# Kernel tuning notes

Measured on AMD Instinct MI355X. Metric: run time of the kernel, lower is better.

The kernel has to match this reference:

```python
import jax, jax.numpy as jnp
import numpy as np

B, S, H, D = 4, 1024, 16, 64


def setup_inputs() -> dict:
    key = jax.random.key(0)
    k1, k2 = jax.random.split(key)
    qkv = jax.random.normal(k1, (B, S, 3, H, D), dtype=jnp.float32)
    bias = jax.random.normal(k2, (1, H, S, S), dtype=jnp.float32)
    return {"qkv": qkv, "bias": bias}


def reference(qkv, bias):
    # flash_attn_qkvpacked_func(qkv, softmax_scale=None -> 1/sqrt(D), bias=bias, causal=False)
    q = qkv[:, :, 0]  # (B, S, H, D)
    k = qkv[:, :, 1]
    v = qkv[:, :, 2]
    scale = 1.0 / jnp.sqrt(jnp.asarray(D, dtype=qkv.dtype))
    # scores: (B, H, S_q, S_k)
    scores = jnp.einsum("bshd,bthd->bhst", q, k) * scale + bias
    probs = jax.nn.softmax(scores, axis=-1)
    out = jnp.einsum("bhst,bthd->bshd", probs, v)  # (B, S, H, D)
    return out
```

## Files before the change

kernel.cpp:

```cpp
#include <hip/hip_runtime.h>

#define NB 4
#define NS 1024
#define NH 16
#define ND 64

typedef __attribute__((ext_vector_type(8))) short bf16x8;
typedef __attribute__((ext_vector_type(4))) float f32x4;

static __device__ __forceinline__ short f2bf(float x) {
  __bf16 h = (__bf16)x;
  return __builtin_bit_cast(short, h);
}
static __device__ __forceinline__ float bf2f(short s) {
  unsigned u = ((unsigned)(unsigned short)s) << 16;
  return __builtin_bit_cast(float, u);
}

__global__ __launch_bounds__(512, 2)
void fsa_fwd(const float* __restrict__ qkv,
             const float* __restrict__ bias,
             float* __restrict__ out)
{
  const int hw = blockIdx.x;
  const int lg = ((hw & 7) << 6) | (hw >> 3);
  const int b  = lg & 3;
  const int qt = (lg >> 2) & 7;
  const int h  = lg >> 5;

  const int tid  = threadIdx.x;
  const int w    = tid >> 6;
  const int lane = tid & 63;
  const int lo   = lane & 15;
  const int hi   = lane >> 4;
  const int q0   = qt * 128;

  __shared__ __attribute__((aligned(16))) short Ksh[64 * 64];
  __shared__ __attribute__((aligned(16))) short VTsh[64 * 64];
  __shared__ __attribute__((aligned(16))) short Psh[8][16 * 64];

  bf16x8 qf[2];
  {
    const int qs = q0 + w * 16 + lo;
    const float* qp = qkv + ((size_t)(b * NS + qs) * 3) * (NH * ND) + h * ND + hi * 8;
    #pragma unroll
    for (int f = 0; f < 2; ++f) {
      float4 x0 = *(const float4*)(qp + f * 32);
      float4 x1 = *(const float4*)(qp + f * 32 + 4);
      float v[8] = {x0.x, x0.y, x0.z, x0.w, x1.x, x1.y, x1.z, x1.w};
      #pragma unroll
      for (int j = 0; j < 8; ++j) qf[f][j] = f2bf(v[j] * 0.125f);
    }
  }

  const size_t tstr = 3 * NH * ND;
  const float* kg = qkv + (size_t)b * NS * tstr + 1 * NH * ND + h * ND;
  const float* vg = qkv + (size_t)b * NS * tstr + 2 * NH * ND + h * ND;

  const int krow = tid >> 3;
  const int kd   = (tid & 7) * 8;
  const int vrow = (tid & 31) * 2;
  const int vd   = (tid >> 5) * 4;

  const float* bb = bias + (size_t)h * NS * NS + (size_t)(q0 + w * 16 + hi * 4) * NS + lo;

  float psum[4] = {0.f, 0.f, 0.f, 0.f};
  f32x4 oacc[4];
  #pragma unroll
  for (int dt = 0; dt < 4; ++dt) { f32x4 z = {0.f, 0.f, 0.f, 0.f}; oacc[dt] = z; }

  for (int it = 0; it < 16; ++it) {
    const int t0 = it * 64;

    bf16x8 w0;
    {
      const float* src = kg + (size_t)(t0 + krow) * tstr + kd;
      float4 a = ((const float4*)src)[0];
      float4 c = ((const float4*)src)[1];
      float v[8] = {a.x,a.y,a.z,a.w, c.x,c.y,c.z,c.w};
      #pragma unroll
      for (int j = 0; j < 8; ++j) w0[j] = f2bf(v[j]);
    }
    unsigned vpk[4];
    {
      const float* s0 = vg + (size_t)(t0 + vrow) * tstr + vd;
      const float* s1 = s0 + tstr;
      float4 a0 = *(const float4*)s0;
      float4 b0 = *(const float4*)s1;
      float r0[4] = {a0.x,a0.y,a0.z,a0.w};
      float r1[4] = {b0.x,b0.y,b0.z,b0.w};
      #pragma unroll
      for (int j = 0; j < 4; ++j)
        vpk[j] = (unsigned)(unsigned short)f2bf(r0[j]) |
                 ((unsigned)(unsigned short)f2bf(r1[j]) << 16);
    }

    __syncthreads();

    {
      const int base = krow * 64 + kd;
      const int sw = (krow & 7) << 3;
      *(bf16x8*)&Ksh[(base ^ sw)] = w0;
    }
    {
      unsigned* vt32 = (unsigned*)VTsh;
      #pragma unroll
      for (int j = 0; j < 4; ++j) {
        const int R = vd + j;
        vt32[R * 32 + ((vrow >> 1) ^ ((R & 7) << 2))] = vpk[j];
      }
    }

    float br[4][4];
    #pragma unroll
    for (int r = 0; r < 4; ++r)
      #pragma unroll
      for (int tt = 0; tt < 4; ++tt)
        br[r][tt] = bb[(size_t)r * NS + t0 + tt * 16];

    __syncthreads();

    __builtin_amdgcn_s_setprio(1);
    f32x4 sacc[4];
    #pragma unroll
    for (int tt = 0; tt < 4; ++tt) {
      f32x4 sb;
      #pragma unroll
      for (int r = 0; r < 4; ++r) sb[r] = br[r][tt] - 8.f;
      const int kr = tt * 16 + lo;
      const int ksw = (kr & 7) << 3;
      bf16x8 k0 = *(const bf16x8*)&Ksh[(kr * 64      + hi * 8) ^ ksw];
      bf16x8 k1 = *(const bf16x8*)&Ksh[(kr * 64 + 32 + hi * 8) ^ ksw];
      sb = __builtin_amdgcn_mfma_f32_16x16x32_bf16(qf[0], k0, sb, 0, 0, 0);
      sb = __builtin_amdgcn_mfma_f32_16x16x32_bf16(qf[1], k1, sb, 0, 0, 0);
      sacc[tt] = sb;
    }

    short* pw = Psh[w];
    #pragma unroll
    for (int r = 0; r < 4; ++r) {
      const int row = hi * 4 + r;
      const int sw = (row & 7) << 3;
      #pragma unroll
      for (int tt = 0; tt < 4; ++tt) {
        float p = __expf(sacc[tt][r]);
        short pb = f2bf(p);
        psum[r] += bf2f(pb);
        pw[row * 64 + ((tt * 16 + lo) ^ sw)] = pb;
      }
    }
    asm volatile("s_waitcnt lgkmcnt(0)" ::: "memory");

    bf16x8 pf0, pf1;
    {
      const int psw = (lo & 7) << 3;
      pf0 = *(const bf16x8*)&pw[lo * 64 + ((     hi * 8) ^ psw)];
      pf1 = *(const bf16x8*)&pw[lo * 64 + ((32 + hi * 8) ^ psw)];
    }
    #pragma unroll
    for (int dt = 0; dt < 4; ++dt) {
      const int vr = dt * 16 + lo;
      const int vsw = (vr & 7) << 3;
      bf16x8 v0 = *(const bf16x8*)&VTsh[vr * 64 + ((     hi * 8) ^ vsw)];
      bf16x8 v1 = *(const bf16x8*)&VTsh[vr * 64 + ((32 + hi * 8) ^ vsw)];
      oacc[dt] = __builtin_amdgcn_mfma_f32_16x16x32_bf16(pf0, v0, oacc[dt], 0, 0, 0);
      oacc[dt] = __builtin_amdgcn_mfma_f32_16x16x32_bf16(pf1, v1, oacc[dt], 0, 0, 0);
    }
    __builtin_amdgcn_s_setprio(0);
  }

  #pragma unroll
  for (int r = 0; r < 4; ++r) {
    psum[r] += __shfl_xor(psum[r], 1, 64);
    psum[r] += __shfl_xor(psum[r], 2, 64);
    psum[r] += __shfl_xor(psum[r], 4, 64);
    psum[r] += __shfl_xor(psum[r], 8, 64);
  }

  float* ob = out + ((size_t)(b * NS + q0 + w * 16 + hi * 4) * NH + h) * ND + lo;
  #pragma unroll
  for (int r = 0; r < 4; ++r) {
    float inv = 1.f / psum[r];
    #pragma unroll
    for (int dt = 0; dt < 4; ++dt)
      ob[(size_t)r * NH * ND + dt * 16] = oacc[dt][r] * inv;
  }
}

extern "C" void kernel_launch(void* const* d_in, const int* in_sizes, int n_in,
                              void* d_out, int out_size, void* d_ws, size_t ws_size,
                              hipStream_t stream) {
  const float* qkv  = (const float*)d_in[0];
  const float* bias = (const float*)d_in[1];
  float* out = (float*)d_out;
  dim3 grid(NB * NH * (NS / 128));
  fsa_fwd<<<grid, 512, 0, stream>>>(qkv, bias, out);
}
```

Measured before the change: 49.22 us.

## Prefetch next K/V and bias tile into registers, switch softmax to exp2

Global loads for the next K/V tile and the next bias tile are now issued into registers during the current iteration, so their latency overlaps the current MFMA and softmax work. Q is prescaled by log2(e) and the bias is scaled the same way, so the exponential becomes a native exp2. The row sum now accumulates fp32 probabilities instead of their bf16-rounded values. This keeps more registers live under launch_bounds(512,2) and slightly changes the rounding of the normalisation.

Measured after the change: 64.67 us. 31.4% more time.

```diff
diff --git a/kernel.cpp b/kernel.cpp
--- a/kernel.cpp
+++ b/kernel.cpp
@@ -1,4 +1,5 @@
 #include <hip/hip_runtime.h>
+#include <cmath>
 
 #define NB 4
 #define NS 1024
@@ -12,10 +13,16 @@
   __bf16 h = (__bf16)x;
   return __builtin_bit_cast(short, h);
 }
-static __device__ __forceinline__ float bf2f(short s) {
-  unsigned u = ((unsigned)(unsigned short)s) << 16;
-  return __builtin_bit_cast(float, u);
-}
+
+static __device__ __forceinline__ float fast_exp2(float x) {
+#if __has_builtin(__builtin_amdgcn_exp2f)
+  return __builtin_amdgcn_exp2f(x);
+#else
+  return exp2f(x);
+#endif
+}
+
+#define LOG2E 1.44269504f
 
 __global__ __launch_bounds__(512, 2)
 void fsa_fwd(const float* __restrict__ qkv,
@@ -49,7 +56,7 @@
       float4 x1 = *(const float4*)(qp + f * 32 + 4);
       float v[8] = {x0.x, x0.y, x0.z, x0.w, x1.x, x1.y, x1.z, x1.w};
       #pragma unroll
-      for (int j = 0; j < 8; ++j) qf[f][j] = f2bf(v[j] * 0.125f);
+      for (int j = 0; j < 8; ++j) qf[f][j] = f2bf(v[j] * (0.125f * LOG2E));
     }
   }
 
@@ -69,71 +76,81 @@
   #pragma unroll
   for (int dt = 0; dt < 4; ++dt) { f32x4 z = {0.f, 0.f, 0.f, 0.f}; oacc[dt] = z; }
 
+  float4 kpa, kpb, vpa, vpb;
+  float br[4][4];
+
+#define LOAD_KV(T0) do { \
+    const float* src_ = kg + (size_t)((T0) + krow) * tstr + kd; \
+    kpa = ((const float4*)src_)[0]; \
+    kpb = ((const float4*)src_)[1]; \
+    const float* s0_ = vg + (size_t)((T0) + vrow) * tstr + vd; \
+    vpa = *(const float4*)s0_; \
+    vpb = *(const float4*)(s0_ + tstr); \
+  } while (0)
+
+#define LOAD_BIAS(T0) do { \
+    _Pragma("unroll") \
+    for (int r_ = 0; r_ < 4; ++r_) { \
+      _Pragma("unroll") \
+      for (int tt_ = 0; tt_ < 4; ++tt_) \
+        br[r_][tt_] = bb[(size_t)r_ * NS + (T0) + tt_ * 16]; \
+    } \
+  } while (0)
+
+#define STAGE() do { \
+    bf16x8 w0_; \
+    { \
+      float v_[8] = {kpa.x,kpa.y,kpa.z,kpa.w, kpb.x,kpb.y,kpb.z,kpb.w}; \
+      _Pragma("unroll") \
+      for (int j_ = 0; j_ < 8; ++j_) w0_[j_] = f2bf(v_[j_]); \
+    } \
+    { \
+      const int base_ = krow * 64 + kd; \
+      const int sw_ = (krow & 7) << 3; \
+      *(bf16x8*)&Ksh[base_ ^ sw_] = w0_; \
+    } \
+    { \
+      float r0_[4] = {vpa.x,vpa.y,vpa.z,vpa.w}; \
+      float r1_[4] = {vpb.x,vpb.y,vpb.z,vpb.w}; \
+      unsigned* vt_ = (unsigned*)VTsh; \
+      _Pragma("unroll") \
+      for (int j_ = 0; j_ < 4; ++j_) { \
+        unsigned pk_ = (unsigned)(unsigned short)f2bf(r0_[j_]) | \
+                       ((unsigned)(unsigned short)f2bf(r1_[j_]) << 16); \
+        const int R_ = vd + j_; \
+        vt_[R_ * 32 + ((vrow >> 1) ^ ((R_ & 7) << 2))] = pk_; \
+      } \
+    } \
+  } while (0)
+
+  LOAD_KV(0);
+  LOAD_BIAS(0);
+
+  #pragma unroll 1
   for (int it = 0; it < 16; ++it) {
-    const int t0 = it * 64;
-
-    bf16x8 w0;
-    {
-      const float* src = kg + (size_t)(t0 + krow) * tstr + kd;
-      float4 a = ((const float4*)src)[0];
-      float4 c = ((const float4*)src)[1];
-      float v[8] = {a.x,a.y,a.z,a.w, c.x,c.y,c.z,c.w};
+    __syncthreads();
+    STAGE();
+    if (it < 15) LOAD_KV((it + 1) * 64);
+    __syncthreads();
+
+    f32x4 sacc[4];
+    #pragma unroll
+    for (int tt = 0; tt < 4; ++tt) {
       #pragma unroll
-      for (int j = 0; j < 8; ++j) w0[j] = f2bf(v[j]);
-    }
-    unsigned vpk[4];
-    {
-      const float* s0 = vg + (size_t)(t0 + vrow) * tstr + vd;
-      const float* s1 = s0 + tstr;
-      float4 a0 = *(const float4*)s0;
-      float4 b0 = *(const float4*)s1;
-      float r0[4] = {a0.x,a0.y,a0.z,a0.w};
-      float r1[4] = {b0.x,b0.y,b0.z,b0.w};
-      #pragma unroll
-      for (int j = 0; j < 4; ++j)
-        vpk[j] = (unsigned)(unsigned short)f2bf(r0[j]) |
-                 ((unsigned)(unsigned short)f2bf(r1[j]) << 16);
-    }
-
-    __syncthreads();
-
-    {
-      const int base = krow * 64 + kd;
-      const int sw = (krow & 7) << 3;
-      *(bf16x8*)&Ksh[(base ^ sw)] = w0;
-    }
-    {
-      unsigned* vt32 = (unsigned*)VTsh;
-      #pragma unroll
-      for (int j = 0; j < 4; ++j) {
-        const int R = vd + j;
-        vt32[R * 32 + ((vrow >> 1) ^ ((R & 7) << 2))] = vpk[j];
-      }
-    }
-
-    float br[4][4];
-    #pragma unroll
-    for (int r = 0; r < 4; ++r)
-      #pragma unroll
-      for (int tt = 0; tt < 4; ++tt)
-        br[r][tt] = bb[(size_t)r * NS + t0 + tt * 16];
-
-    __syncthreads();
+      for (int r = 0; r < 4; ++r)
+        sacc[tt][r] = br[r][tt] * LOG2E - (8.f * LOG2E);
+    }
+    if (it < 15) LOAD_BIAS((it + 1) * 64);
 
     __builtin_amdgcn_s_setprio(1);
-    f32x4 sacc[4];
     #pragma unroll
     for (int tt = 0; tt < 4; ++tt) {
-      f32x4 sb;
-      #pragma unroll
-      for (int r = 0; r < 4; ++r) sb[r] = br[r][tt] - 8.f;
       const int kr = tt * 16 + lo;
       const int ksw = (kr & 7) << 3;
       bf16x8 k0 = *(const bf16x8*)&Ksh[(kr * 64      + hi * 8) ^ ksw];
       bf16x8 k1 = *(const bf16x8*)&Ksh[(kr * 64 + 32 + hi * 8) ^ ksw];
-      sb = __builtin_amdgcn_mfma_f32_16x16x32_bf16(qf[0], k0, sb, 0, 0, 0);
-      sb = __builtin_amdgcn_mfma_f32_16x16x32_bf16(qf[1], k1, sb, 0, 0, 0);
-      sacc[tt] = sb;
+      sacc[tt] = __builtin_amdgcn_mfma_f32_16x16x32_bf16(qf[0], k0, sacc[tt], 0, 0, 0);
+      sacc[tt] = __builtin_amdgcn_mfma_f32_16x16x32_bf16(qf[1], k1, sacc[tt], 0, 0, 0);
     }
 
     short* pw = Psh[w];
@@ -143,10 +160,9 @@
       const int sw = (row & 7) << 3;
       #pragma unroll
       for (int tt = 0; tt < 4; ++tt) {
-        float p = __expf(sacc[tt][r]);
-        short pb = f2bf(p);
-        psum[r] += bf2f(pb);
-        pw[row * 64 + ((tt * 16 + lo) ^ sw)] = pb;
+        float p = fast_exp2(sacc[tt][r]);
+        psum[r] += p;
+        pw[row * 64 + ((tt * 16 + lo) ^ sw)] = f2bf(p);
       }
     }
     asm volatile("s_waitcnt lgkmcnt(0)" ::: "memory");
@@ -168,6 +184,10 @@
     }
     __builtin_amdgcn_s_setprio(0);
   }
+
+#undef STAGE
+#undef LOAD_BIAS
+#undef LOAD_KV
 
   #pragma unroll
   for (int r = 0; r < 4; ++r) {
```

## Use 1024-thread blocks with 256-query tiles and exp2-based softmax

Applied to the files above, without the earlier changes.

Doubles the query tile per block from 128 to 256 rows with 16 waves, so each staged K/V tile in shared memory is reused by twice as many waves. The per-block K/V load work is split across more threads, and the grid shrinks to 256 blocks. The softmax now uses a native exp2 with log2e folded into the Q scale and the bias FMA. The row sum accumulates the unrounded fp32 probability rather than the bf16-rounded value. Fewer blocks (256 on 256 CUs) and larger barriers risk worse latency hiding, and launch_bounds(1024,4) may pressure registers.

After: 50.51 us. 1.03x slower.

```diff
diff --git a/kernel.cpp b/kernel.cpp
--- a/kernel.cpp
+++ b/kernel.cpp
@@ -1,43 +1,50 @@
 #include <hip/hip_runtime.h>
+#include <cmath>
 
 #define NB 4
 #define NS 1024
 #define NH 16
 #define ND 64
+#define LOG2E 1.44269504f
 
 typedef __attribute__((ext_vector_type(8))) short bf16x8;
+typedef __attribute__((ext_vector_type(4))) short bf16x4;
 typedef __attribute__((ext_vector_type(4))) float f32x4;
 
 static __device__ __forceinline__ short f2bf(float x) {
   __bf16 h = (__bf16)x;
   return __builtin_bit_cast(short, h);
 }
-static __device__ __forceinline__ float bf2f(short s) {
-  unsigned u = ((unsigned)(unsigned short)s) << 16;
-  return __builtin_bit_cast(float, u);
-}
-
-__global__ __launch_bounds__(512, 2)
+
+static __device__ __forceinline__ float fast_exp2(float x) {
+#if __has_builtin(__builtin_amdgcn_exp2f)
+  return __builtin_amdgcn_exp2f(x);
+#else
+  return exp2f(x);
+#endif
+}
+
+__global__ __launch_bounds__(1024, 4)
 void fsa_fwd(const float* __restrict__ qkv,
              const float* __restrict__ bias,
              float* __restrict__ out)
 {
   const int hw = blockIdx.x;
-  const int lg = ((hw & 7) << 6) | (hw >> 3);
+  const int lg = ((hw & 7) << 5) | (hw >> 3);
   const int b  = lg & 3;
-  const int qt = (lg >> 2) & 7;
-  const int h  = lg >> 5;
+  const int qt = (lg >> 2) & 3;
+  const int h  = lg >> 4;
 
   const int tid  = threadIdx.x;
   const int w    = tid >> 6;
   const int lane = tid & 63;
   const int lo   = lane & 15;
   const int hi   = lane >> 4;
-  const int q0   = qt * 128;
+  const int q0   = qt * 256;
 
   __shared__ __attribute__((aligned(16))) short Ksh[64 * 64];
   __shared__ __attribute__((aligned(16))) short VTsh[64 * 64];
-  __shared__ __attribute__((aligned(16))) short Psh[8][16 * 64];
+  __shared__ __attribute__((aligned(16))) short Psh[16][16 * 64];
 
   bf16x8 qf[2];
   {
@@ -49,7 +56,7 @@
       float4 x1 = *(const float4*)(qp + f * 32 + 4);
       float v[8] = {x0.x, x0.y, x0.z, x0.w, x1.x, x1.y, x1.z, x1.w};
       #pragma unroll
-      for (int j = 0; j < 8; ++j) qf[f][j] = f2bf(v[j] * 0.125f);
+      for (int j = 0; j < 8; ++j) qf[f][j] = f2bf(v[j] * (0.125f * LOG2E));
     }
   }
 
@@ -57,10 +64,10 @@
   const float* kg = qkv + (size_t)b * NS * tstr + 1 * NH * ND + h * ND;
   const float* vg = qkv + (size_t)b * NS * tstr + 2 * NH * ND + h * ND;
 
-  const int krow = tid >> 3;
-  const int kd   = (tid & 7) * 8;
+  const int krow = tid >> 4;
+  const int kd   = (tid & 15) * 4;
   const int vrow = (tid & 31) * 2;
-  const int vd   = (tid >> 5) * 4;
+  const int vd   = (tid >> 5) * 2;
 
   const float* bb = bias + (size_t)h * NS * NS + (size_t)(q0 + w * 16 + hi * 4) * NS + lo;
 
@@ -69,30 +76,26 @@
   #pragma unroll
   for (int dt = 0; dt < 4; ++dt) { f32x4 z = {0.f, 0.f, 0.f, 0.f}; oacc[dt] = z; }
 
+  #pragma unroll 1
   for (int it = 0; it < 16; ++it) {
     const int t0 = it * 64;
 
-    bf16x8 w0;
+    bf16x4 kw;
     {
       const float* src = kg + (size_t)(t0 + krow) * tstr + kd;
-      float4 a = ((const float4*)src)[0];
-      float4 c = ((const float4*)src)[1];
-      float v[8] = {a.x,a.y,a.z,a.w, c.x,c.y,c.z,c.w};
-      #pragma unroll
-      for (int j = 0; j < 8; ++j) w0[j] = f2bf(v[j]);
-    }
-    unsigned vpk[4];
+      float4 a = *(const float4*)src;
+      float v[4] = {a.x, a.y, a.z, a.w};
+      #pragma unroll
+      for (int j = 0; j < 4; ++j) kw[j] = f2bf(v[j]);
+    }
+    unsigned vpk[2];
     {
       const float* s0 = vg + (size_t)(t0 + vrow) * tstr + vd;
       const float* s1 = s0 + tstr;
-      float4 a0 = *(const float4*)s0;
-      float4 b0 = *(const float4*)s1;
-      float r0[4] = {a0.x,a0.y,a0.z,a0.w};
-      float r1[4] = {b0.x,b0.y,b0.z,b0.w};
-      #pragma unroll
-      for (int j = 0; j < 4; ++j)
-        vpk[j] = (unsigned)(unsigned short)f2bf(r0[j]) |
-                 ((unsigned)(unsigned short)f2bf(r1[j]) << 16);
+      float2 a0 = *(const float2*)s0;
+      float2 b0 = *(const float2*)s1;
+      vpk[0] = (unsigned)(unsigned short)f2bf(a0.x) | ((unsigned)(unsigned short)f2bf(b0.x) << 16);
+      vpk[1] = (unsigned)(unsigned short)f2bf(a0.y) | ((unsigned)(unsigned short)f2bf(b0.y) << 16);
     }
 
     __syncthreads();
@@ -100,12 +103,12 @@
     {
       const int base = krow * 64 + kd;
       const int sw = (krow & 7) << 3;
-      *(bf16x8*)&Ksh[(base ^ sw)] = w0;
+      *(bf16x4*)&Ksh[base ^ sw] = kw;
     }
     {
       unsigned* vt32 = (unsigned*)VTsh;
       #pragma unroll
-      for (int j = 0; j < 4; ++j) {
+      for (int j = 0; j < 2; ++j) {
         const int R = vd + j;
         vt32[R * 32 + ((vrow >> 1) ^ ((R & 7) << 2))] = vpk[j];
       }
@@ -126,7 +129,7 @@
     for (int tt = 0; tt < 4; ++tt) {
       f32x4 sb;
       #pragma unroll
-      for (int r = 0; r < 4; ++r) sb[r] = br[r][tt] - 8.f;
+      for (int r = 0; r < 4; ++r) sb[r] = fmaf(br[r][tt], LOG2E, -8.f * LOG2E);
       const int kr = tt * 16 + lo;
       const int ksw = (kr & 7) << 3;
       bf16x8 k0 = *(const bf16x8*)&Ksh[(kr * 64      + hi * 8) ^ ksw];
@@ -143,10 +146,9 @@
       const int sw = (row & 7) << 3;
       #pragma unroll
       for (int tt = 0; tt < 4; ++tt) {
-        float p = __expf(sacc[tt][r]);
-        short pb = f2bf(p);
-        psum[r] += bf2f(pb);
-        pw[row * 64 + ((tt * 16 + lo) ^ sw)] = pb;
+        float p = fast_exp2(sacc[tt][r]);
+        psum[r] += p;
+        pw[row * 64 + ((tt * 16 + lo) ^ sw)] = f2bf(p);
       }
     }
     asm volatile("s_waitcnt lgkmcnt(0)" ::: "memory");
@@ -193,6 +195,6 @@
   const float* qkv  = (const float*)d_in[0];
   const float* bias = (const float*)d_in[1];
   float* out = (float*)d_out;
-  dim3 grid(NB * NH * (NS / 128));
-  fsa_fwd<<<grid, 512, 0, stream>>>(qkv, bias, out);
-}
+  dim3 grid(NB * NH * (NS / 256));
+  fsa_fwd<<<grid, 1024, 0, stream>>>(qkv, bias, out);
+}
```

## Transpose score MFMA so bias loads vectorize and P stores pack

Applied to the files above, without the earlier changes.

Swaps the MFMA operands so the score tile comes out transposed: each lane holds four consecutive key columns for one query row. Bias can then be read with float4 loads, P is written to LDS as packed 4-short stores, and each lane keeps one row sum that is reduced with two shuffles. The log2e factor is folded into the Q scale and bias so exp2 replaces __expf. Row sums now accumulate the fp32 probabilities rather than their bf16-rounded values, which slightly changes numerics.

After: 60.48 us. 1.23x slower.

```diff
diff --git a/kernel.cpp b/kernel.cpp
--- a/kernel.cpp
+++ b/kernel.cpp
@@ -1,20 +1,27 @@
 #include <hip/hip_runtime.h>
+#include <cmath>
 
 #define NB 4
 #define NS 1024
 #define NH 16
 #define ND 64
+#define LOG2E 1.44269504f
 
 typedef __attribute__((ext_vector_type(8))) short bf16x8;
+typedef __attribute__((ext_vector_type(4))) short short4v;
 typedef __attribute__((ext_vector_type(4))) float f32x4;
 
 static __device__ __forceinline__ short f2bf(float x) {
   __bf16 h = (__bf16)x;
   return __builtin_bit_cast(short, h);
 }
-static __device__ __forceinline__ float bf2f(short s) {
-  unsigned u = ((unsigned)(unsigned short)s) << 16;
-  return __builtin_bit_cast(float, u);
+
+static __device__ __forceinline__ float fast_exp2(float x) {
+#if __has_builtin(__builtin_amdgcn_exp2f)
+  return __builtin_amdgcn_exp2f(x);
+#else
+  return exp2f(x);
+#endif
 }
 
 __global__ __launch_bounds__(512, 2)
@@ -49,7 +56,7 @@
       float4 x1 = *(const float4*)(qp + f * 32 + 4);
       float v[8] = {x0.x, x0.y, x0.z, x0.w, x1.x, x1.y, x1.z, x1.w};
       #pragma unroll
-      for (int j = 0; j < 8; ++j) qf[f][j] = f2bf(v[j] * 0.125f);
+      for (int j = 0; j < 8; ++j) qf[f][j] = f2bf(v[j] * (0.125f * LOG2E));
     }
   }
 
@@ -62,13 +69,14 @@
   const int vrow = (tid & 31) * 2;
   const int vd   = (tid >> 5) * 4;
 
-  const float* bb = bias + (size_t)h * NS * NS + (size_t)(q0 + w * 16 + hi * 4) * NS + lo;
-
-  float psum[4] = {0.f, 0.f, 0.f, 0.f};
+  const float* bbT = bias + (size_t)h * NS * NS + (size_t)(q0 + w * 16 + lo) * NS + hi * 4;
+
+  float psum = 0.f;
   f32x4 oacc[4];
   #pragma unroll
   for (int dt = 0; dt < 4; ++dt) { f32x4 z = {0.f, 0.f, 0.f, 0.f}; oacc[dt] = z; }
 
+  #pragma unroll 1
   for (int it = 0; it < 16; ++it) {
     const int t0 = it * 64;
 
@@ -100,7 +108,7 @@
     {
       const int base = krow * 64 + kd;
       const int sw = (krow & 7) << 3;
-      *(bf16x8*)&Ksh[(base ^ sw)] = w0;
+      *(bf16x8*)&Ksh[base ^ sw] = w0;
     }
     {
       unsigned* vt32 = (unsigned*)VTsh;
@@ -111,12 +119,10 @@
       }
     }
 
-    float br[4][4];
-    #pragma unroll
-    for (int r = 0; r < 4; ++r)
-      #pragma unroll
-      for (int tt = 0; tt < 4; ++tt)
-        br[r][tt] = bb[(size_t)r * NS + t0 + tt * 16];
+    float4 brT[4];
+    #pragma unroll
+    for (int tt = 0; tt < 4; ++tt)
+      brT[tt] = *(const float4*)(bbT + t0 + tt * 16);
 
     __syncthreads();
 
@@ -126,27 +132,29 @@
     for (int tt = 0; tt < 4; ++tt) {
       f32x4 sb;
       #pragma unroll
-      for (int r = 0; r < 4; ++r) sb[r] = br[r][tt] - 8.f;
+      for (int r = 0; r < 4; ++r) sb[r] = fmaf(brT[tt][r], LOG2E, -8.f * LOG2E);
       const int kr = tt * 16 + lo;
       const int ksw = (kr & 7) << 3;
-      bf16x8 k0 = *(const bf16x8*)&Ksh[(kr * 64      + hi * 8) ^ ksw];
-      bf16x8 k1 = *(const bf16x8*)&Ksh[(kr * 64 + 32 + hi * 8) ^ ksw];
-      sb = __builtin_amdgcn_mfma_f32_16x16x32_bf16(qf[0], k0, sb, 0, 0, 0);
-      sb = __builtin_amdgcn_mfma_f32_16x16x32_bf16(qf[1], k1, sb, 0, 0, 0);
+      bf16x8 a0 = *(const bf16x8*)&Ksh[(kr * 64      + hi * 8) ^ ksw];
+      bf16x8 a1 = *(const bf16x8*)&Ksh[(kr * 64 + 32 + hi * 8) ^ ksw];
+      sb = __builtin_amdgcn_mfma_f32_16x16x32_bf16(a0, qf[0], sb, 0, 0, 0);
+      sb = __builtin_amdgcn_mfma_f32_16x16x32_bf16(a1, qf[1], sb, 0, 0, 0);
       sacc[tt] = sb;
     }
 
     short* pw = Psh[w];
-    #pragma unroll
-    for (int r = 0; r < 4; ++r) {
-      const int row = hi * 4 + r;
-      const int sw = (row & 7) << 3;
+    {
+      const int psw = (lo & 7) << 3;
       #pragma unroll
       for (int tt = 0; tt < 4; ++tt) {
-        float p = __expf(sacc[tt][r]);
-        short pb = f2bf(p);
-        psum[r] += bf2f(pb);
-        pw[row * 64 + ((tt * 16 + lo) ^ sw)] = pb;
+        short4v pk;
+        #pragma unroll
+        for (int r = 0; r < 4; ++r) {
+          float p = fast_exp2(sacc[tt][r]);
+          psum += p;
+          pk[r] = f2bf(p);
+        }
+        *(short4v*)&pw[lo * 64 + ((tt * 16 + hi * 4) ^ psw)] = pk;
       }
     }
     asm volatile("s_waitcnt lgkmcnt(0)" ::: "memory");
@@ -169,18 +177,13 @@
     __builtin_amdgcn_s_setprio(0);
   }
 
-  #pragma unroll
-  for (int r = 0; r < 4; ++r) {
-    psum[r] += __shfl_xor(psum[r], 1, 64);
-    psum[r] += __shfl_xor(psum[r], 2, 64);
-    psum[r] += __shfl_xor(psum[r], 4, 64);
-    psum[r] += __shfl_xor(psum[r], 8, 64);
-  }
+  psum += __shfl_xor(psum, 16, 64);
+  psum += __shfl_xor(psum, 32, 64);
 
   float* ob = out + ((size_t)(b * NS + q0 + w * 16 + hi * 4) * NH + h) * ND + lo;
   #pragma unroll
   for (int r = 0; r < 4; ++r) {
-    float inv = 1.f / psum[r];
+    const float inv = 1.f / __shfl(psum, hi * 4 + r, 64);
     #pragma unroll
     for (int dt = 0; dt < 4; ++dt)
       ob[(size_t)r * NH * ND + dt * 16] = oacc[dt][r] * inv;
```
